# Kernel tuning notes

Measured on AMD Instinct MI355X. Metric: run time of the kernel, lower is better.

Reference implementation:

```python
import jax, jax.numpy as jnp
import numpy as np

N, E, H, C, G = 10000, 20000, 12, 768, 64  # nodes, edges, heads, per-head dim, graphs
NEG_SLOPE = 0.2


def _gat_layer(x, W, a_src, a_dst, b, src, dst):
    # x: [N, 768], W: [768, H*C], a_src/a_dst: [H, C], b: [C]
    h = (x @ W).reshape(-1, H, C)                      # [N, H, C]
    s = jnp.einsum('nhc,hc->nh', h, a_src)             # alpha_src per node
    d = jnp.einsum('nhc,hc->nh', h, a_dst)             # alpha_dst per node
    e = jax.nn.leaky_relu(s[src] + d[dst], NEG_SLOPE)  # [Etot, H]
    # segment softmax over incoming edges of each destination node
    m = jax.lax.stop_gradient(jax.ops.segment_max(e, dst, num_segments=N))
    ex = jnp.exp(e - m[dst])
    den = jax.ops.segment_sum(ex, dst, num_segments=N)
    alpha = ex / (den[dst] + 1e-16)                    # [Etot, H]
    out = jax.ops.segment_sum(h[src] * alpha[:, :, None], dst, num_segments=N)
    return out.mean(axis=1) + b                        # concat=False -> head mean, [N, C]


def setup_inputs() -> dict:
    key = jax.random.key(0)
    ks = jax.random.split(key, 16)
    sc = 0.02
    f32 = jnp.float32
    return {
        'x': jax.random.normal(ks[0], (N, 768), f32),
        'edge_index': jax.random.randint(ks[1], (2, E), 0, N),
        'batch': jnp.sort(jax.random.randint(ks[2], (N,), 0, G)),
        'W1': (jax.random.normal(ks[3], (768, H * C), f32) * sc),
        'a_src1': (jax.random.normal(ks[4], (H, C), f32) * sc),
        'a_dst1': (jax.random.normal(ks[5], (H, C), f32) * sc),
        'b1': jnp.zeros((C,), f32),
        'W2': (jax.random.normal(ks[6], (768, H * C), f32) * sc),
        'a_src2': (jax.random.normal(ks[7], (H, C), f32) * sc),
        'a_dst2': (jax.random.normal(ks[8], (H, C), f32) * sc),
        'b2': jnp.zeros((C,), f32),
        'mlp_w1': (jax.random.normal(ks[9], (768, 128), f32) * sc),
        'mlp_b1': jnp.zeros((128,), f32),
        'mlp_w2': (jax.random.normal(ks[10], (128, 4), f32) * sc),
        'mlp_b2': jnp.zeros((4,), f32),
    }


def reference(x, edge_index, batch, W1, a_src1, a_dst1, b1, W2, a_src2, a_dst2, b2,
              mlp_w1, mlp_b1, mlp_w2, mlp_b2):
    loops = jnp.arange(N)                               # GATConv add_self_loops=True
    src = jnp.concatenate([edge_index[0], loops])
    dst = jnp.concatenate([edge_index[1], loops])
    h = _gat_layer(x, W1, a_src1, a_dst1, b1, src, dst)
    h = _gat_layer(h, W2, a_src2, a_dst2, b2, src, dst)
    # scatter_mean over graph assignment
    ssum = jax.ops.segment_sum(h, batch, num_segments=G)
    cnt = jax.ops.segment_sum(jnp.ones((N,), h.dtype), batch, num_segments=G)
    g = ssum / jnp.maximum(cnt, 1.0)[:, None]           # [G, 768]
    z = jax.nn.relu(g @ mlp_w1 + mlp_b1)
    return z @ mlp_w2 + mlp_b2                          # [G, 4] logits
```

## Files before the change

### kernel.cpp

```cpp
#include <hip/hip_runtime.h>
#include <stdint.h>

typedef unsigned short u16;
typedef unsigned int   u32;

#define NNODES 10000
#define NEDGES 20000
#define ETOT   30000
#define NHEADS 12
#define CDIM   768
#define FDIM   768
#define KDIM   9216
#define NGRAPH 64
#define MPAD   10240
#define NEG_SLOPE 0.2f
#define DMAX   32

typedef __attribute__((ext_vector_type(8))) short short8;
typedef __attribute__((ext_vector_type(4))) float f32x4;

__device__ __forceinline__ u16 f32_bf16(float f) {
  u32 u = __float_as_uint(f);
  u = (u + 0x7FFFu + ((u >> 16) & 1u)) >> 16;
  return (u16)u;
}
__device__ __forceinline__ float bf16_f32(u16 v) {
  return __uint_as_float(((u32)v) << 16);
}

__global__ void k_count(const int* __restrict__ dste, int* __restrict__ counts) {
  int e = blockIdx.x * blockDim.x + threadIdx.x;
  if (e >= ETOT) return;
  int dst;
  if (e < NEDGES) dst = dste[e]; else dst = e - NEDGES;
  atomicAdd(&counts[dst], 1);
}

__global__ void k_scan(const int* __restrict__ counts, int* __restrict__ offs) {
  __shared__ int part[256];
  int t = threadIdx.x;
  const int chunk = 40;
  int beg = t * chunk;
  int end = beg + chunk; if (end > NNODES) end = NNODES;
  int s = 0;
  for (int i = beg; i < end && i < NNODES; i++) s += counts[i];
  part[t] = s;
  __syncthreads();
  for (int d = 1; d < 256; d <<= 1) {
    int v = (t >= d) ? part[t - d] : 0;
    __syncthreads();
    part[t] += v;
    __syncthreads();
  }
  int base = (t == 0) ? 0 : part[t - 1];
  for (int i = beg; i < end && i < NNODES; i++) { offs[i] = base; base += counts[i]; }
  if (t == 255) offs[NNODES] = base;
}

__global__ void k_seed(const int* __restrict__ offs, int* __restrict__ cursor) {
  int n = blockIdx.x * blockDim.x + threadIdx.x;
  if (n < NNODES) cursor[n] = offs[n];
}

__global__ void k_scatter(const int* __restrict__ dste, int* __restrict__ cursor,
                          int* __restrict__ elist) {
  int e = blockIdx.x * blockDim.x + threadIdx.x;
  if (e >= ETOT) return;
  int dst;
  if (e < NEDGES) dst = dste[e]; else dst = e - NEDGES;
  int pos = atomicAdd(&cursor[dst], 1);
  elist[pos] = e;
}

__global__ void k_U(const float* __restrict__ W, const float* __restrict__ a_src,
                    const float* __restrict__ a_dst, float* __restrict__ Ut) {
  int k = blockIdx.x;
  int t = threadIdx.x, w = t >> 6, l = t & 63;
  const float* Wrow = W + (size_t)k * KDIM;
#pragma unroll
  for (int q = 0; q < 6; q++) {
    int o = w * 6 + q;
    int h = (o < 12) ? o : o - 12;
    const float* av = (o < 12) ? (a_src + h * CDIM) : (a_dst + h * CDIM);
    const float* wr = Wrow + h * CDIM;
    float p = 0.f;
    for (int c = l; c < CDIM; c += 64) p += wr[c] * av[c];
#pragma unroll
    for (int d = 32; d > 0; d >>= 1) p += __shfl_down(p, d, 64);
    if (l == 0) Ut[o * FDIM + k] = p;
  }
}

__global__ void k_sd(const float* __restrict__ xin, const float* __restrict__ Ut,
                     float* __restrict__ sd) {
  __shared__ float UtS[24 * FDIM];
  int t = threadIdx.x, w = t >> 6, l = t & 63;
  const float4* U4 = (const float4*)Ut;
  float4* S4 = (float4*)UtS;
  for (int i = t; i < 24 * FDIM / 4; i += 256) S4[i] = U4[i];
  __syncthreads();
#pragma unroll
  for (int rep = 0; rep < 5; rep++) {
    int n = blockIdx.x * 20 + w * 5 + rep;
    if (n >= NNODES) continue;
    const float* xr = xin + (size_t)n * FDIM;
    float4 x0 = *(const float4*)(xr + 4 * l);
    float4 x1 = *(const float4*)(xr + 4 * l + 256);
    float4 x2 = *(const float4*)(xr + 4 * l + 512);
#pragma unroll
    for (int o = 0; o < 24; o++) {
      const float4* up = (const float4*)(UtS + o * FDIM + 4 * l);
      float4 u0 = up[0];
      float4 u1 = up[64];
      float4 u2 = up[128];
      float a = x0.x * u0.x + x0.y * u0.y + x0.z * u0.z + x0.w * u0.w
              + x1.x * u1.x + x1.y * u1.y + x1.z * u1.z + x1.w * u1.w
              + x2.x * u2.x + x2.y * u2.y + x2.z * u2.z + x2.w * u2.w;
#pragma unroll
      for (int d = 32; d > 0; d >>= 1) a += __shfl_xor(a, d, 64);
      if (l == 0) sd[n * 24 + o] = a;
    }
  }
}

__global__ void k_trans2(const float* __restrict__ W, u16* __restrict__ Bt2) {
  int kt = blockIdx.x * 32, jt = blockIdx.y * 32;
  int tx = threadIdx.x, ty = threadIdx.y;
  __shared__ float tile[32][33];
  int h0 = jt / 768, c0 = jt - h0 * 768;
#pragma unroll
  for (int r = 0; r < 4; r++)
    tile[ty + 8 * r][tx] = W[(size_t)(kt + ty + 8 * r) * KDIM + jt + tx];
  __syncthreads();
#pragma unroll
  for (int r = 0; r < 4; r++)
    Bt2[(size_t)(c0 + ty + 8 * r) * KDIM + h0 * 768 + kt + tx] = f32_bf16(tile[tx][ty + 8 * r]);
}

__global__ void k_agg(const float* __restrict__ xin, const int* __restrict__ ei,
                      const int* __restrict__ offs, const int* __restrict__ elist,
                      const float* __restrict__ sd, u16* __restrict__ y) {
  int t = threadIdx.x, w = t >> 6, l = t & 63;
  int n = blockIdx.x * 4 + w;
  __shared__ int   srcsS[4][DMAX];
  __shared__ float alphS[4][NHEADS * DMAX];
  if (n >= NNODES) return;
  int* srcs = srcsS[w];
  float* alph = alphS[w];
  int beg = offs[n];
  int deg = offs[n + 1] - beg;
  if (deg > DMAX) deg = DMAX;
  if (l < deg) {
    int e = elist[beg + l];
    srcs[l] = (e < NEDGES) ? ei[e] : e - NEDGES;
  }
  __builtin_amdgcn_wave_barrier();
  for (int p = l; p < deg * NHEADS; p += 64) {
    int i = p / NHEADS, h = p - i * NHEADS;
    float v = sd[srcs[i] * 24 + h] + sd[n * 24 + 12 + h];
    v = (v > 0.f) ? v : NEG_SLOPE * v;
    alph[h * DMAX + i] = v;
  }
  __builtin_amdgcn_wave_barrier();
  if (l < NHEADS) {
    float m = -1e30f;
    for (int i = 0; i < deg; i++) m = fmaxf(m, alph[l * DMAX + i]);
    float s = 0.f;
    for (int i = 0; i < deg; i++) {
      float ex = expf(alph[l * DMAX + i] - m);
      alph[l * DMAX + i] = ex;
      s += ex;
    }
    float inv = 1.f / (s + 1e-16f);
    for (int i = 0; i < deg; i++) alph[l * DMAX + i] *= inv;
  }
  __builtin_amdgcn_wave_barrier();
#pragma unroll
  for (int pass = 0; pass < 3; pass++) {
    float4 acc12[NHEADS];
#pragma unroll
    for (int h = 0; h < NHEADS; h++) acc12[h] = make_float4(0.f, 0.f, 0.f, 0.f);
    for (int i = 0; i < deg; i++) {
      float4 xs = *(const float4*)(xin + (size_t)srcs[i] * FDIM + pass * 256 + 4 * l);
#pragma unroll
      for (int h = 0; h < NHEADS; h++) {
        float a = alph[h * DMAX + i];
        acc12[h].x += a * xs.x;
        acc12[h].y += a * xs.y;
        acc12[h].z += a * xs.z;
        acc12[h].w += a * xs.w;
      }
    }
    u16* yr = y + (size_t)n * KDIM + pass * 256 + 4 * l;
#pragma unroll
    for (int h = 0; h < NHEADS; h++) {
      ushort4 pv;
      pv.x = f32_bf16(acc12[h].x);
      pv.y = f32_bf16(acc12[h].y);
      pv.z = f32_bf16(acc12[h].z);
      pv.w = f32_bf16(acc12[h].w);
      *(ushort4*)(yr + h * CDIM) = pv;
    }
  }
}

#define GLL16(G, L) __builtin_amdgcn_global_load_lds( \
  (const __attribute__((address_space(1))) void*)(G), \
  (__attribute__((address_space(3))) void*)(L), 16, 0, 0)

__global__ __launch_bounds__(512, 2) void k_gemm2(const u16* __restrict__ A,
    const u16* __restrict__ B, float* __restrict__ C0, float* __restrict__ C1) {
  __shared__ __align__(16) u16 As[2][256 * 64];
  __shared__ __align__(16) u16 Bs[2][256 * 64];
  int t = threadIdx.x;
  int w = t >> 6, l = t & 63;
  int bid = blockIdx.x;
  int xcd = bid & 7, j = bid >> 3;
  int p = j / 6, rem = j - p * 6;
  int ks = rem / 3, cx = rem - ks * 3;
  int by = xcd * 5 + p;
  int row0 = by * 256, col0 = cx * 256;
  int kbase = ks * (KDIM / 2);
  int wr = w >> 2, wc = w & 3;
  int lr = l & 15;
  int koff = (l >> 4) * 16;
  int swzr = (lr & 7) << 4;
  int rb = t >> 3;
  int csw = ((t & 7) ^ (rb & 7)) * 8;
  const u16* baseA = A + (size_t)(row0 + rb) * KDIM + kbase + csw;
  const u16* baseB = B + (size_t)(col0 + rb) * KDIM + kbase + csw;

  f32x4 acc[8][4] = {};
  short8 a[4][2], b0[2][2], b1[2][2];

  auto stA = [&](int buf, int h, int s) {
    const u16* g = baseA + (size_t)(h * 128) * KDIM + s * 64;
    u16* lp = (u16*)&As[buf][0] + h * 8192 + (w << 9);
    GLL16(g, lp);
    GLL16(g + (size_t)64 * KDIM, lp + 4096);
  };
  auto stB = [&](int buf, int h, int s) {
    const u16* g = baseB + (size_t)(h * 128) * KDIM + s * 64;
    u16* lp = (u16*)&Bs[buf][0] + h * 8192 + (w << 9);
    GLL16(g, lp);
    GLL16(g + (size_t)64 * KDIM, lp + 4096);
  };
  auto ldA = [&](int buf, int mo) {
#pragma unroll
    for (int m = 0; m < 4; m++)
#pragma unroll
      for (int c = 0; c < 2; c++) {
        int row = wr * 128 + (mo + m) * 16 + lr;
        int off = row * 128 + ((c * 64 + koff) ^ swzr);
        a[m][c] = *(const short8*)((const char*)&As[buf][0] + off);
      }
  };
  auto ldB = [&](int buf, short8 (*bb)[2], int no) {
#pragma unroll
    for (int n = 0; n < 2; n++)
#pragma unroll
      for (int c = 0; c < 2; c++) {
        int row = wc * 64 + (no + n) * 16 + lr;
        int off = row * 128 + ((c * 64 + koff) ^ swzr);
        bb[n][c] = *(const short8*)((const char*)&Bs[buf][0] + off);
      }
  };
  auto mm8 = [&](short8 (*bb)[2], int mo, int no) {
    __builtin_amdgcn_s_setprio(1);
#pragma unroll
    for (int m = 0; m < 4; m++)
#pragma unroll
      for (int n = 0; n < 2; n++)
#pragma unroll
        for (int c = 0; c < 2; c++)
          acc[mo + m][no + n] = __builtin_amdgcn_mfma_f32_16x16x32_bf16(
              a[m][c], bb[n][c], acc[mo + m][no + n], 0, 0, 0);
    __builtin_amdgcn_s_setprio(0);
  };

  stA(0, 0, 0); stA(0, 1, 0); stB(0, 0, 0); stB(0, 1, 0);
  stB(1, 0, 1); stA(1, 0, 1);
  asm volatile("s_waitcnt vmcnt(4)" ::: "memory");
  __builtin_amdgcn_s_barrier();

  const int NIT = KDIM / 2 / 64;
  for (int s = 0; s < NIT; s++) {
    int P = s & 1;
    ldA(P, 0); ldB(P, b0, 0);
    if (s + 1 < NIT) stB(P ^ 1, 1, s + 1);
    __builtin_amdgcn_s_barrier();
    mm8(b0, 0, 0);
    __builtin_amdgcn_s_barrier();
    ldB(P, b1, 2);
    if (s + 1 < NIT) stA(P ^ 1, 1, s + 1);
    __builtin_amdgcn_s_barrier();
    mm8(b1, 0, 2);
    __builtin_amdgcn_s_barrier();
    ldA(P, 4);
    if (s + 2 < NIT) stB(P, 0, s + 2);
    __builtin_amdgcn_s_barrier();
    mm8(b1, 4, 2);
    __builtin_amdgcn_s_barrier();
    if (s + 2 < NIT) stA(P, 0, s + 2);
    __builtin_amdgcn_s_barrier();
    mm8(b0, 4, 0);
    if (s < NIT - 1) {
      if (s <= NIT - 3) asm volatile("s_waitcnt vmcnt(4)" ::: "memory");
      else              asm volatile("s_waitcnt vmcnt(0)" ::: "memory");
    }
    __builtin_amdgcn_s_barrier();
  }

  float* Cd = ks ? C1 : C0;
  int lg = l >> 4;
#pragma unroll
  for (int m = 0; m < 8; m++)
#pragma unroll
    for (int n = 0; n < 4; n++) {
      int col = col0 + wc * 64 + n * 16 + lr;
#pragma unroll
      for (int r = 0; r < 4; r++) {
        int row = row0 + wr * 128 + m * 16 + lg * 4 + r;
        if (row < NNODES)
          Cd[(size_t)row * FDIM + col] = acc[m][n][r];
      }
    }
}

__global__ void k_red(const float* __restrict__ p1, const float* __restrict__ bias,
                      float* __restrict__ io) {
  int e = (blockIdx.x * 256 + threadIdx.x) * 4;
  float4 a = *(const float4*)(io + e);
  float4 b = *(const float4*)(p1 + e);
  float4 bv = *(const float4*)(bias + (e % FDIM));
  const float sc = 1.f / 12.f;
  float4 o;
  o.x = (a.x + b.x) * sc + bv.x;
  o.y = (a.y + b.y) * sc + bv.y;
  o.z = (a.z + b.z) * sc + bv.z;
  o.w = (a.w + b.w) * sc + bv.w;
  *(float4*)(io + e) = o;
}

__global__ void k_pool(const float* __restrict__ h2, const int* __restrict__ batch,
                       float* __restrict__ g) {
  int gi = blockIdx.x;
  int c = blockIdx.y * 256 + threadIdx.x;
  int lo = 0, hi = NNODES;
  while (lo < hi) { int mid = (lo + hi) >> 1; if (batch[mid] < gi) lo = mid + 1; else hi = mid; }
  int start = lo;
  lo = start; hi = NNODES;
  while (lo < hi) { int mid = (lo + hi) >> 1; if (batch[mid] < gi + 1) lo = mid + 1; else hi = mid; }
  int end = lo;
  int cnt = end - start; if (cnt < 1) cnt = 1;
  float inv = 1.f / (float)cnt;
  float s = 0.f;
  for (int n = start; n < end; n++) s += h2[(size_t)n * FDIM + c];
  g[gi * FDIM + c] = s * inv;
}

__global__ void k_mlp(const float* __restrict__ g, const float* __restrict__ w1,
                      const float* __restrict__ b1, const float* __restrict__ w2,
                      const float* __restrict__ b2, float* __restrict__ out) {
  int gi = blockIdx.x;
  int t = threadIdx.x;
  __shared__ float gs[FDIM];
  __shared__ float zs[128];
  for (int i = t; i < FDIM; i += 128) gs[i] = g[gi * FDIM + i];
  __syncthreads();
  float a = b1[t];
  for (int k = 0; k < FDIM; k++) a += gs[k] * w1[k * 128 + t];
  zs[t] = (a > 0.f) ? a : 0.f;
  __syncthreads();
  if (t < 4) {
    float o = b2[t];
    for (int i = 0; i < 128; i++) o += zs[i] * w2[i * 4 + t];
    out[gi * 4 + t] = o;
  }
}

extern "C" void kernel_launch(void* const* d_in, const int* in_sizes, int n_in,
                              void* d_out, int out_size, void* d_ws, size_t ws_size,
                              hipStream_t stream) {
  const float* x    = (const float*)d_in[0];
  const int*   ei   = (const int*)d_in[1];
  const int*   batch= (const int*)d_in[2];
  const float* W1   = (const float*)d_in[3];
  const float* as1  = (const float*)d_in[4];
  const float* ad1  = (const float*)d_in[5];
  const float* b1   = (const float*)d_in[6];
  const float* W2   = (const float*)d_in[7];
  const float* as2  = (const float*)d_in[8];
  const float* ad2  = (const float*)d_in[9];
  const float* b2   = (const float*)d_in[10];
  const float* mw1  = (const float*)d_in[11];
  const float* mb1  = (const float*)d_in[12];
  const float* mw2  = (const float*)d_in[13];
  const float* mb2  = (const float*)d_in[14];
  float* out = (float*)d_out;
  (void)in_sizes; (void)n_in; (void)out_size; (void)ws_size;

  char* wsb = (char*)d_ws;
  size_t off = 0;
  auto alloc = [&](size_t bytes) -> void* {
    void* p = wsb + off;
    off += (bytes + 255) & ~(size_t)255;
    return p;
  };
  u16*  y      = (u16*)alloc((size_t)MPAD * KDIM * 2);
  u16*  Bt2    = (u16*)alloc((size_t)FDIM * KDIM * 2);
  float* h1    = (float*)alloc((size_t)NNODES * FDIM * 4);
  float* h2    = (float*)alloc((size_t)NNODES * FDIM * 4);
  float* sd    = (float*)alloc((size_t)NNODES * 24 * 4);
  float* Ut    = (float*)alloc((size_t)FDIM * 24 * 4);
  int*  counts = (int*)alloc((size_t)NNODES * 4);
  int*  offs   = (int*)alloc((size_t)(NNODES + 1) * 4);
  int*  cursor = (int*)alloc((size_t)NNODES * 4);
  int*  elist  = (int*)alloc((size_t)ETOT * 4);
  float* gbuf  = (float*)alloc((size_t)NGRAPH * FDIM * 4);

  hipMemsetAsync(counts, 0, NNODES * 4, stream);
  hipMemsetAsync(y + (size_t)NNODES * KDIM, 0, (size_t)(MPAD - NNODES) * KDIM * 2, stream);
  k_count<<<(ETOT + 255) / 256, 256, 0, stream>>>(ei + NEDGES, counts);
  k_scan<<<1, 256, 0, stream>>>(counts, offs);
  k_seed<<<(NNODES + 255) / 256, 256, 0, stream>>>(offs, cursor);
  k_scatter<<<(ETOT + 255) / 256, 256, 0, stream>>>(ei + NEDGES, cursor, elist);

  for (int layer = 0; layer < 2; layer++) {
    const float* xin  = layer ? h1  : x;
    const float* W    = layer ? W2  : W1;
    const float* asrc = layer ? as2 : as1;
    const float* adst = layer ? ad2 : ad1;
    const float* bb   = layer ? b2  : b1;
    float* hout       = layer ? h2  : h1;
    float* cpart      = layer ? h1  : h2;

    k_U<<<FDIM, 256, 0, stream>>>(W, asrc, adst, Ut);
    k_sd<<<(NNODES + 19) / 20, 256, 0, stream>>>(xin, Ut, sd);
    k_trans2<<<dim3(FDIM / 32, KDIM / 32), dim3(32, 8), 0, stream>>>(W, Bt2);
    k_agg<<<(NNODES + 3) / 4, 256, 0, stream>>>(xin, ei, offs, elist, sd, y);
    k_gemm2<<<240, 512, 0, stream>>>(y, Bt2, hout, cpart);
    k_red<<<NNODES * FDIM / 1024, 256, 0, stream>>>(cpart, bb, hout);
  }

  k_pool<<<dim3(NGRAPH, 3), 256, 0, stream>>>(h2, batch, gbuf);
  k_mlp<<<NGRAPH, 128, 0, stream>>>(gbuf, mw1, mb1, mw2, mb2, out);
}
```

Baseline: 894.8 us.

## Store GEMM operands in K-plane blocked layout and shrink GEMM tiles

Rewrites the aggregated activation y and the transposed weight Bt2 into 64-wide K-plane blocks, so each GEMM K-step reads one contiguous plane instead of strided rows. The GEMM tile drops from 256x256 with K=64 to 256x128 with K=32, using half the LDS. This permits 4 blocks per CU and launches 480 blocks instead of 240. A small kernel now zero-fills the padded rows in each plane in place of one memset. Smaller tiles reduce per-block data reuse, and the loop runs twice as many K-steps with several barriers each.

Measured after the change: 901.1 us. About the same (+0.7%).

```diff
diff --git a/kernel.cpp b/kernel.cpp
--- a/kernel.cpp
+++ b/kernel.cpp
@@ -15,6 +15,7 @@
 #define MPAD   10240
 #define NEG_SLOPE 0.2f
 #define DMAX   32
+#define NPLANE 144
 
 typedef __attribute__((ext_vector_type(8))) short short8;
 typedef __attribute__((ext_vector_type(4))) float f32x4;
@@ -124,17 +125,29 @@
 }
 
 __global__ void k_trans2(const float* __restrict__ W, u16* __restrict__ Bt2) {
-  int kt = blockIdx.x * 32, jt = blockIdx.y * 32;
+  int kb = blockIdx.x * 32, jt = blockIdx.y * 32;
   int tx = threadIdx.x, ty = threadIdx.y;
   __shared__ float tile[32][33];
   int h0 = jt / 768, c0 = jt - h0 * 768;
+  int plane = (h0 * 768 + kb) >> 6;
 #pragma unroll
   for (int r = 0; r < 4; r++)
-    tile[ty + 8 * r][tx] = W[(size_t)(kt + ty + 8 * r) * KDIM + jt + tx];
+    tile[ty + 8 * r][tx] = W[(size_t)(kb + ty + 8 * r) * KDIM + jt + tx];
   __syncthreads();
 #pragma unroll
   for (int r = 0; r < 4; r++)
-    Bt2[(size_t)(c0 + ty + 8 * r) * KDIM + h0 * 768 + kt + tx] = f32_bf16(tile[tx][ty + 8 * r]);
+    Bt2[(size_t)plane * (768 * 64) + (size_t)(c0 + ty + 8 * r) * 64 + ((kb + tx) & 63)]
+        = f32_bf16(tile[tx][ty + 8 * r]);
+}
+
+__global__ void k_zpad(u16* __restrict__ y) {
+  int idx = blockIdx.x * 256 + threadIdx.x;
+  if (idx >= NPLANE * (MPAD - NNODES) * 8) return;
+  int e = idx * 8;
+  int plane = e / ((MPAD - NNODES) * 64);
+  int rem = e - plane * ((MPAD - NNODES) * 64);
+  u16* p = y + (size_t)plane * (MPAD * 64) + (size_t)NNODES * 64 + rem;
+  *(short8*)p = (short8){0, 0, 0, 0, 0, 0, 0, 0};
 }
 
 __global__ void k_agg(const float* __restrict__ xin, const int* __restrict__ ei,
@@ -175,6 +188,7 @@
     for (int i = 0; i < deg; i++) alph[l * DMAX + i] *= inv;
   }
   __builtin_amdgcn_wave_barrier();
+  int lg = l >> 4, lo16 = l & 15;
 #pragma unroll
   for (int pass = 0; pass < 3; pass++) {
     float4 acc12[NHEADS];
@@ -191,7 +205,6 @@
         acc12[h].w += a * xs.w;
       }
     }
-    u16* yr = y + (size_t)n * KDIM + pass * 256 + 4 * l;
 #pragma unroll
     for (int h = 0; h < NHEADS; h++) {
       ushort4 pv;
@@ -199,7 +212,8 @@
       pv.y = f32_bf16(acc12[h].y);
       pv.z = f32_bf16(acc12[h].z);
       pv.w = f32_bf16(acc12[h].w);
-      *(ushort4*)(yr + h * CDIM) = pv;
+      int plane = h * 12 + pass * 4 + lg;
+      *(ushort4*)(y + (size_t)plane * (MPAD * 64) + (size_t)n * 64 + 4 * lo16) = pv;
     }
   }
 }
@@ -208,119 +222,107 @@
   (const __attribute__((address_space(1))) void*)(G), \
   (__attribute__((address_space(3))) void*)(L), 16, 0, 0)
 
-__global__ __launch_bounds__(512, 2) void k_gemm2(const u16* __restrict__ A,
+__global__ __launch_bounds__(512, 4) void k_gemm2(const u16* __restrict__ A,
     const u16* __restrict__ B, float* __restrict__ C0, float* __restrict__ C1) {
-  __shared__ __align__(16) u16 As[2][256 * 64];
-  __shared__ __align__(16) u16 Bs[2][256 * 64];
+  __shared__ __align__(16) u16 As[2][256 * 32];
+  __shared__ __align__(16) u16 Bs[2][128 * 32];
   int t = threadIdx.x;
   int w = t >> 6, l = t & 63;
   int bid = blockIdx.x;
   int xcd = bid & 7, j = bid >> 3;
-  int p = j / 6, rem = j - p * 6;
-  int ks = rem / 3, cx = rem - ks * 3;
-  int by = xcd * 5 + p;
-  int row0 = by * 256, col0 = cx * 256;
-  int kbase = ks * (KDIM / 2);
-  int wr = w >> 2, wc = w & 3;
-  int lr = l & 15;
-  int koff = (l >> 4) * 16;
-  int swzr = (lr & 7) << 4;
-  int rb = t >> 3;
-  int csw = ((t & 7) ^ (rb & 7)) * 8;
-  const u16* baseA = A + (size_t)(row0 + rb) * KDIM + kbase + csw;
-  const u16* baseB = B + (size_t)(col0 + rb) * KDIM + kbase + csw;
-
-  f32x4 acc[8][4] = {};
-  short8 a[4][2], b0[2][2], b1[2][2];
-
-  auto stA = [&](int buf, int h, int s) {
-    const u16* g = baseA + (size_t)(h * 128) * KDIM + s * 64;
-    u16* lp = (u16*)&As[buf][0] + h * 8192 + (w << 9);
-    GLL16(g, lp);
-    GLL16(g + (size_t)64 * KDIM, lp + 4096);
-  };
-  auto stB = [&](int buf, int h, int s) {
-    const u16* g = baseB + (size_t)(h * 128) * KDIM + s * 64;
-    u16* lp = (u16*)&Bs[buf][0] + h * 8192 + (w << 9);
-    GLL16(g, lp);
-    GLL16(g + (size_t)64 * KDIM, lp + 4096);
-  };
-  auto ldA = [&](int buf, int mo) {
-#pragma unroll
-    for (int m = 0; m < 4; m++)
-#pragma unroll
-      for (int c = 0; c < 2; c++) {
-        int row = wr * 128 + (mo + m) * 16 + lr;
-        int off = row * 128 + ((c * 64 + koff) ^ swzr);
-        a[m][c] = *(const short8*)((const char*)&As[buf][0] + off);
-      }
-  };
-  auto ldB = [&](int buf, short8 (*bb)[2], int no) {
-#pragma unroll
-    for (int n = 0; n < 2; n++)
-#pragma unroll
-      for (int c = 0; c < 2; c++) {
-        int row = wc * 64 + (no + n) * 16 + lr;
-        int off = row * 128 + ((c * 64 + koff) ^ swzr);
-        bb[n][c] = *(const short8*)((const char*)&Bs[buf][0] + off);
-      }
-  };
-  auto mm8 = [&](short8 (*bb)[2], int mo, int no) {
+  int p = j / 12, rem = j - p * 12;
+  int ks = rem / 6, cx = rem - ks * 6;
+  int row0 = (xcd * 5 + p) * 256, col0 = cx * 128;
+  int K0b = ks * NPLANE;
+  int wr = w >> 1, wc = w & 1;
+  int lr = l & 15, lg = l >> 4;
+  int koff = lg * 16;
+  int swzr = (lr & 3) << 4;
+  int rb = t >> 2;
+  int csw = ((t & 3) ^ (rb & 3)) * 8;
+
+  f32x4 acc[4][4] = {};
+  short8 alo[2], ahi[2], blo[2], bhi[2];
+
+  auto stA = [&](int buf, int h, int K0) {
+    int kt2 = K0 >> 1, hf = (K0 & 1) * 32;
+    const u16* g = A + (size_t)kt2 * (MPAD * 64)
+                     + (size_t)(row0 + h * 128 + rb) * 64 + hf + csw;
+    GLL16(g, (u16*)&As[buf][0] + h * 4096 + (w << 9));
+  };
+  auto stB = [&](int buf, int K0) {
+    int kt2 = K0 >> 1, hf = (K0 & 1) * 32;
+    const u16* g = B + (size_t)kt2 * (768 * 64)
+                     + (size_t)(col0 + rb) * 64 + hf + csw;
+    GLL16(g, (u16*)&Bs[buf][0] + (w << 9));
+  };
+  auto ldA = [&](int buf, short8* d, int mo) {
+#pragma unroll
+    for (int m = 0; m < 2; m++) {
+      int row = wr * 64 + (mo + m) * 16 + lr;
+      d[m] = *(const short8*)((const char*)&As[buf][0] + row * 64 + (koff ^ swzr));
+    }
+  };
+  auto ldB = [&](int buf, short8* d, int no) {
+#pragma unroll
+    for (int n = 0; n < 2; n++) {
+      int row = wc * 64 + (no + n) * 16 + lr;
+      d[n] = *(const short8*)((const char*)&Bs[buf][0] + row * 64 + (koff ^ swzr));
+    }
+  };
+  auto mm4 = [&](short8* aa, short8* bb, int mo, int no) {
     __builtin_amdgcn_s_setprio(1);
 #pragma unroll
-    for (int m = 0; m < 4; m++)
+    for (int m = 0; m < 2; m++)
 #pragma unroll
       for (int n = 0; n < 2; n++)
-#pragma unroll
-        for (int c = 0; c < 2; c++)
-          acc[mo + m][no + n] = __builtin_amdgcn_mfma_f32_16x16x32_bf16(
-              a[m][c], bb[n][c], acc[mo + m][no + n], 0, 0, 0);
+        acc[mo + m][no + n] = __builtin_amdgcn_mfma_f32_16x16x32_bf16(
+            aa[m], bb[n], acc[mo + m][no + n], 0, 0, 0);
     __builtin_amdgcn_s_setprio(0);
   };
 
-  stA(0, 0, 0); stA(0, 1, 0); stB(0, 0, 0); stB(0, 1, 0);
-  stB(1, 0, 1); stA(1, 0, 1);
-  asm volatile("s_waitcnt vmcnt(4)" ::: "memory");
+  stB(0, K0b); stA(0, 0, K0b); stA(0, 1, K0b);
+  stB(1, K0b + 1); stA(1, 0, K0b + 1);
+  asm volatile("s_waitcnt vmcnt(2)" ::: "memory");
   __builtin_amdgcn_s_barrier();
 
-  const int NIT = KDIM / 2 / 64;
+  const int NIT = NPLANE;
   for (int s = 0; s < NIT; s++) {
     int P = s & 1;
-    ldA(P, 0); ldB(P, b0, 0);
-    if (s + 1 < NIT) stB(P ^ 1, 1, s + 1);
-    __builtin_amdgcn_s_barrier();
-    mm8(b0, 0, 0);
-    __builtin_amdgcn_s_barrier();
-    ldB(P, b1, 2);
-    if (s + 1 < NIT) stA(P ^ 1, 1, s + 1);
-    __builtin_amdgcn_s_barrier();
-    mm8(b1, 0, 2);
-    __builtin_amdgcn_s_barrier();
-    ldA(P, 4);
-    if (s + 2 < NIT) stB(P, 0, s + 2);
-    __builtin_amdgcn_s_barrier();
-    mm8(b1, 4, 2);
-    __builtin_amdgcn_s_barrier();
-    if (s + 2 < NIT) stA(P, 0, s + 2);
-    __builtin_amdgcn_s_barrier();
-    mm8(b0, 4, 0);
+    int K0 = K0b + s;
+    ldA(P, alo, 0); ldB(P, blo, 0);
+    __builtin_amdgcn_s_barrier();
+    mm4(alo, blo, 0, 0);
+    __builtin_amdgcn_s_barrier();
+    ldB(P, bhi, 2);
+    if (s + 1 < NIT) stA(P ^ 1, 1, K0 + 1);
+    __builtin_amdgcn_s_barrier();
+    mm4(alo, bhi, 0, 2);
+    __builtin_amdgcn_s_barrier();
+    ldA(P, ahi, 2);
+    if (s + 2 < NIT) stB(P, K0 + 2);
+    __builtin_amdgcn_s_barrier();
+    mm4(ahi, bhi, 2, 2);
+    __builtin_amdgcn_s_barrier();
+    if (s + 2 < NIT) stA(P, 0, K0 + 2);
+    __builtin_amdgcn_s_barrier();
+    mm4(ahi, blo, 2, 0);
     if (s < NIT - 1) {
-      if (s <= NIT - 3) asm volatile("s_waitcnt vmcnt(4)" ::: "memory");
+      if (s <= NIT - 3) asm volatile("s_waitcnt vmcnt(2)" ::: "memory");
       else              asm volatile("s_waitcnt vmcnt(0)" ::: "memory");
     }
     __builtin_amdgcn_s_barrier();
   }
 
   float* Cd = ks ? C1 : C0;
-  int lg = l >> 4;
-#pragma unroll
-  for (int m = 0; m < 8; m++)
+#pragma unroll
+  for (int m = 0; m < 4; m++)
 #pragma unroll
     for (int n = 0; n < 4; n++) {
       int col = col0 + wc * 64 + n * 16 + lr;
 #pragma unroll
       for (int r = 0; r < 4; r++) {
-        int row = row0 + wr * 128 + m * 16 + lg * 4 + r;
+        int row = row0 + wr * 64 + m * 16 + lg * 4 + r;
         if (row < NNODES)
           Cd[(size_t)row * FDIM + col] = acc[m][n][r];
       }
@@ -420,7 +422,7 @@
   float* gbuf  = (float*)alloc((size_t)NGRAPH * FDIM * 4);
 
   hipMemsetAsync(counts, 0, NNODES * 4, stream);
-  hipMemsetAsync(y + (size_t)NNODES * KDIM, 0, (size_t)(MPAD - NNODES) * KDIM * 2, stream);
+  k_zpad<<<(NPLANE * (MPAD - NNODES) * 8 + 255) / 256, 256, 0, stream>>>(y);
   k_count<<<(ETOT + 255) / 256, 256, 0, stream>>>(ei + NEDGES, counts);
   k_scan<<<1, 256, 0, stream>>>(counts, offs);
   k_seed<<<(NNODES + 255) / 256, 256, 0, stream>>>(offs, cursor);
@@ -439,7 +441,7 @@
     k_sd<<<(NNODES + 19) / 20, 256, 0, stream>>>(xin, Ut, sd);
     k_trans2<<<dim3(FDIM / 32, KDIM / 32), dim3(32, 8), 0, stream>>>(W, Bt2);
     k_agg<<<(NNODES + 3) / 4, 256, 0, stream>>>(xin, ei, offs, elist, sd, y);
-    k_gemm2<<<240, 512, 0, stream>>>(y, Bt2, hout, cpart);
+    k_gemm2<<<480, 512, 0, stream>>>(y, Bt2, hout, cpart);
     k_red<<<NNODES * FDIM / 1024, 256, 0, stream>>>(cpart, bb, hout);
   }
 
```
